# Kernel optimization log

Measured on AMD Instinct MI355X. Metric: run time of the kernel, lower is better.

Reference implementation:

```python
import jax, jax.numpy as jnp
import numpy as np

N = 8192; S = 32; EMB = 256; NH = 8; HD = EMB // NH; NT = 4; K = 2; L = 2; E = 131072
IN_DIMS = [128, 64, 32, 16]; COUNTS = [4096, 2048, 1024, 1024]
BETA = 1.0; TEMPER = 1.0; SLOPE = 0.2; LN_EPS = 1e-5


def setup_inputs() -> dict:
    key = jax.random.key(0)
    ks = iter(jax.random.split(key, 64))
    def nrm(shape, scale=1.0):
        return jax.random.normal(next(ks), shape, jnp.float32) * scale
    inp = {}
    for i, (d, c) in enumerate(zip(IN_DIMS, COUNTS)):
        inp[f"feat{i}"] = nrm((c, d))
        inp[f"Wfc{i}"] = nrm((d, EMB), d ** -0.5)
        inp[f"bfc{i}"] = nrm((EMB,), 0.01)
    inp["type_emb"] = nrm((NT, NT))
    inp["Wgcn"] = nrm((K, EMB, EMB), EMB ** -0.5)
    inp["bgcn"] = nrm((K, EMB), 0.01)
    inp["Wre"] = nrm((K, NT, NT), NT ** -0.5)
    inp["bre"] = nrm((K, NT), 0.01)
    inp["wtre"] = jnp.ones((K, NT), jnp.float32)
    inp["Wl"] = nrm((L, EMB, EMB), EMB ** -0.5)
    inp["Wr"] = nrm((L, EMB, EMB), EMB ** -0.5)
    inp["al"] = nrm((L, HD), HD ** -0.5)
    inp["ar"] = nrm((L, HD), HD ** -0.5)
    inp["Wrs"] = nrm((L, NT, NT * NH), NT ** -0.5)
    inp["Wrt"] = nrm((L, NT, NT * NH), NT ** -0.5)
    inp["Wfin"] = nrm((L, EMB, EMB), EMB ** -0.5)
    inp["ln_g"] = jnp.ones((L, EMB), jnp.float32)
    inp["ln_b"] = jnp.zeros((L, EMB), jnp.float32)
    inp["src"] = jax.random.randint(next(ks), (E,), 0, N)
    inp["dst"] = jax.random.randint(next(ks), (E,), 0, N)
    inp["node_type"] = jnp.concatenate([jnp.full((c,), t, jnp.int32) for t, c in enumerate(COUNTS)])
    inp["seqs"] = jax.random.randint(next(ks), (N, S), 0, N)
    return inp


def _l2n(x):
    return x / jnp.maximum(jnp.linalg.norm(x, axis=1, keepdims=True), 1e-12)


def _ln(x, g, b):
    m = x.mean(-1, keepdims=True)
    v = ((x - m) ** 2).mean(-1, keepdims=True)
    return (x - m) * jax.lax.rsqrt(v + LN_EPS) * g + b


def _agt(h, rh, Wl_, Wr_, al_, ar_, Wrs_, Wrt_, Wfin_, g_, b_):
    B, Sq, _ = h.shape
    fl = (h @ Wl_).reshape(B, Sq, NH, HD).transpose(0, 2, 1, 3)  # [B,NH,S,HD]
    fr = (h @ Wr_).reshape(B, Sq, NH, HD).transpose(0, 2, 1, 3)
    sl = jnp.einsum('bhsd,d->bhs', jax.nn.leaky_relu(fl, SLOPE), al_)
    sr = jnp.einsum('bhsd,d->bhs', jax.nn.leaky_relu(fr, SLOPE), ar_)
    score = sl[:, :, :, None] + sr[:, :, None, :]  # [B,NH,S,S]
    rk = (rh @ Wrs_).reshape(B, Sq, NH, NT).transpose(0, 2, 1, 3)  # [B,NH,S,NT]
    rq = (rh @ Wrt_).reshape(B, Sq, NH, NT).transpose(0, 2, 1, 3)
    score = score + BETA * jnp.einsum('bhir,bhjr->bhij', rk, rq)
    attn = jax.nn.softmax(score / TEMPER, axis=-1)
    ctx = jnp.einsum('bhij,bhjd->bhid', attn, fr)
    h_sa = ctx.transpose(0, 2, 1, 3).reshape(B, Sq, EMB)
    return _ln(h + h_sa @ Wfin_, g_, b_)


def reference(feat0, feat1, feat2, feat3, Wfc0, bfc0, Wfc1, bfc1, Wfc2, bfc2, Wfc3, bfc3,
              type_emb, Wgcn, bgcn, Wre, bre, wtre, Wl, Wr, al, ar, Wrs, Wrt, Wfin, ln_g, ln_b,
              src, dst, node_type, seqs):
    feats = [feat0, feat1, feat2, feat3]
    Wfcs = [Wfc0, Wfc1, Wfc2, Wfc3]
    bfcs = [bfc0, bfc1, bfc2, bfc3]
    gh = jnp.concatenate([f @ W + b for f, W, b in zip(feats, Wfcs, bfcs)], axis=0)  # [N,EMB]
    Nn = gh.shape[0]
    loop = jnp.arange(Nn, dtype=src.dtype)  # self-loops (graph.add_self_loop)
    src_f = jnp.concatenate([src, loop]); dst_f = jnp.concatenate([dst, loop])
    ones = jnp.ones(src_f.shape[0], jnp.float32)
    outdeg = jnp.clip(jax.ops.segment_sum(ones, src_f, num_segments=Nn), 1.0)
    indeg = jnp.clip(jax.ops.segment_sum(ones, dst_f, num_segments=Nn), 1.0)
    n_out = outdeg ** -0.5; n_in = indeg ** -0.5
    ret = [_l2n(gh)]
    R = type_emb[node_type]  # [N,NT]
    for k in range(K):
        # GraphConv, norm='both', relu
        x = (gh * n_out[:, None]) @ Wgcn[k]
        gh = jax.nn.relu(jax.ops.segment_sum(x[src_f], dst_f, num_segments=Nn) * n_in[:, None] + bgcn[k])
        # REConv: left norm, weight, per-node type scale, scatter-sum, right norm, bias, relu
        r = ((R * n_out[:, None]) @ Wre[k]) * wtre[k][node_type][:, None]
        R = jax.nn.relu(jax.ops.segment_sum(r[src_f], dst_f, num_segments=Nn) * n_in[:, None] + bre[k])
    h = gh[seqs]   # [N,S,EMB]
    rh = R[seqs]   # [N,S,NT]
    for l in range(L):
        h = _agt(h, rh, Wl[l], Wr[l], al[l], ar[l], Wrs[l], Wrt[l], Wfin[l], ln_g[l], ln_b[l])
        ret.append(_l2n(h[:, 0, :]))
    return jnp.concatenate(ret, axis=1)  # [N, EMB*(1+L)]
```

## Files before the change

kernel.cpp:

```cpp
#include <hip/hip_runtime.h>
#include <hip/hip_bf16.h>
#include <cstdint>
#include <cstddef>

typedef unsigned short ushortT;
typedef unsigned int uintT;

using bf16x8 = __attribute__((ext_vector_type(8))) short;
using f32x4  = __attribute__((ext_vector_type(4))) float;

static constexpr int NN  = 8192;
static constexpr int EE  = 131072;
static constexpr float SLOPE  = 0.2f;
static constexpr float LN_EPS = 1e-5f;

#define DEVI __device__ __forceinline__

DEVI float red32(float v) {
  #pragma unroll
  for (int m = 16; m >= 1; m >>= 1) v += __shfl_xor(v, m, 64);
  return v;
}
DEVI float red64(float v) {
  #pragma unroll
  for (int m = 32; m >= 1; m >>= 1) v += __shfl_xor(v, m, 64);
  return v;
}
DEVI float max32(float v) {
  #pragma unroll
  for (int m = 16; m >= 1; m >>= 1) v = fmaxf(v, __shfl_xor(v, m, 64));
  return v;
}
DEVI float blo(uintT u) { union { uintT i; float f; } c; c.i = u << 16; return c.f; }
DEVI float bhi(uintT u) { union { uintT i; float f; } c; c.i = u & 0xffff0000u; return c.f; }
DEVI float b2f(ushortT u) { union { uintT i; float f; } c; c.i = ((uintT)u) << 16; return c.f; }
DEVI ushortT f2bu(float f) {
  __hip_bfloat16 h = __float2bfloat16(f);
  return *reinterpret_cast<ushortT*>(&h);
}
DEVI void storeC(float* p, float v) { *p = v; }
DEVI void storeC(ushortT* p, float v) { *p = f2bu(v); }

__global__ __launch_bounds__(256) void fc_kernel(
    const float* __restrict__ f0, const float* __restrict__ f1,
    const float* __restrict__ f2, const float* __restrict__ f3,
    const float* __restrict__ w0, const float* __restrict__ w1,
    const float* __restrict__ w2, const float* __restrict__ w3,
    const float* __restrict__ b0, const float* __restrict__ b1,
    const float* __restrict__ b2, const float* __restrict__ b3,
    float* __restrict__ gh, float* __restrict__ out)
{
  const int nb = blockIdx.x * 32;
  const int t  = threadIdx.x;
  int base, D;
  const float *F, *W, *Bv;
  if (nb < 4096)      { base = 0;    D = 128; F = f0; W = w0; Bv = b0; }
  else if (nb < 6144) { base = 4096; D = 64;  F = f1; W = w1; Bv = b1; }
  else if (nb < 7168) { base = 6144; D = 32;  F = f2; W = w2; Bv = b2; }
  else                { base = 7168; D = 16;  F = f3; W = w3; Bv = b3; }

  __shared__ float Fs[32 * 128];
  __shared__ float red[32][4];
  __shared__ float nrm[32];

  const int total = 32 * D;
  for (int i = t; i < total; i += 256) Fs[i] = F[(size_t)(nb - base) * D + i];
  __syncthreads();

  float acc[32];
  #pragma unroll
  for (int r = 0; r < 32; ++r) acc[r] = Bv[t];
  for (int d = 0; d < D; ++d) {
    float w = W[(size_t)d * 256 + t];
    #pragma unroll
    for (int r = 0; r < 32; ++r) acc[r] = fmaf(Fs[r * D + d], w, acc[r]);
  }

  const int lane = t & 63, wid = t >> 6;
  #pragma unroll
  for (int r = 0; r < 32; ++r) {
    float v = acc[r] * acc[r];
    for (int o = 32; o > 0; o >>= 1) v += __shfl_down(v, o, 64);
    if (lane == 0) red[r][wid] = v;
  }
  __syncthreads();
  if (t < 32) {
    float s = red[t][0] + red[t][1] + red[t][2] + red[t][3];
    nrm[t] = 1.0f / fmaxf(sqrtf(s), 1e-12f);
  }
  __syncthreads();
  #pragma unroll
  for (int r = 0; r < 32; ++r) {
    gh[(size_t)(nb + r) * 256 + t]  = acc[r];
    out[(size_t)(nb + r) * 768 + t] = acc[r] * nrm[r];
  }
}

__global__ __launch_bounds__(256) void zero_counts(int* outc, int* inc) {
  int g = blockIdx.x * 256 + threadIdx.x;
  if (g < NN) outc[g] = 0; else inc[g - NN] = 0;
}
__global__ __launch_bounds__(256) void count_deg(const int* __restrict__ src,
                                                 const int* __restrict__ dst,
                                                 int* outc, int* inc) {
  int g = blockIdx.x * 256 + threadIdx.x;
  atomicAdd(&outc[src[g]], 1);
  atomicAdd(&inc[dst[g]], 1);
}
__global__ __launch_bounds__(256) void norm_kernel(const int* __restrict__ outc,
                                                   const int* __restrict__ inc,
                                                   float* n_out, float* n_in) {
  int g = blockIdx.x * 256 + threadIdx.x;
  n_out[g] = rsqrtf((float)outc[g] + 1.0f);
  n_in[g]  = rsqrtf((float)inc[g] + 1.0f);
}
__global__ __launch_bounds__(1024) void scan_kernel(const int* __restrict__ inc,
                                                    int* __restrict__ offs) {
  __shared__ int sums[1024];
  const int t = threadIdx.x;
  int x[8];
  const int base = t * 8;
  int s = 0;
  #pragma unroll
  for (int i = 0; i < 8; ++i) { int v = inc[base + i] + 1; x[i] = s; s += v; }
  sums[t] = s;
  __syncthreads();
  for (int off = 1; off < 1024; off <<= 1) {
    int a = (t >= off) ? sums[t - off] : 0;
    __syncthreads();
    sums[t] += a;
    __syncthreads();
  }
  const int pre = (t > 0) ? sums[t - 1] : 0;
  #pragma unroll
  for (int i = 0; i < 8; ++i) offs[base + i] = pre + x[i];
  if (t == 1023) offs[NN] = sums[1023];
}
__global__ __launch_bounds__(256) void copy_cur(const int* __restrict__ offs, int* cur) {
  int g = blockIdx.x * 256 + threadIdx.x;
  cur[g] = offs[g];
}
__global__ __launch_bounds__(256) void fill_csr(const int* __restrict__ src,
                                                const int* __restrict__ dst,
                                                int* cur, int* __restrict__ csr) {
  int g = blockIdx.x * 256 + threadIdx.x;
  int s, d;
  if (g < EE) { s = src[g]; d = dst[g]; }
  else        { s = g - EE; d = g - EE; }
  int pos = atomicAdd(&cur[d], 1);
  csr[pos] = s;
}
__global__ __launch_bounds__(256) void init_R(const float* __restrict__ type_emb,
                                              const int* __restrict__ nt,
                                              float* __restrict__ R) {
  int g = blockIdx.x * 256 + threadIdx.x;
  int n = g >> 2, c = g & 3;
  R[g] = type_emb[nt[n] * 4 + c];
}

template<bool ROWSCALE, bool STORE, bool RED, typename CT>
__global__ __launch_bounds__(256) void gemm64_kernel(
    const float* __restrict__ A,
    const float* __restrict__ W,
    const float* __restrict__ rowscale,
    CT* __restrict__ C,
    const float* __restrict__ avec,
    float* __restrict__ SSo)
{
  const int m0 = blockIdx.x * 64;
  const int n0 = blockIdx.y * 64;
  const int t  = threadIdx.x;
  const int tr = t & 15, tc = t >> 4;
  __shared__ alignas(16) float As[32][68];
  __shared__ alignas(16) float Bs[32][68];
  __shared__ float red[64][2];
  float acc[4][4] = {};

  for (int ks = 0; ks < 8; ++ks) {
    const int k0 = ks * 32;
    #pragma unroll
    for (int rep = 0; rep < 8; ++rep) {
      int flat = rep * 256 + t;
      int r = flat >> 5, c = flat & 31;
      As[c][r] = A[(size_t)(m0 + r) * 256 + (k0 + c)];
      int rb = flat >> 6, cb = flat & 63;
      Bs[rb][cb] = W[(size_t)(k0 + rb) * 256 + (n0 + cb)];
    }
    __syncthreads();
    #pragma unroll
    for (int k = 0; k < 32; ++k) {
      const float4 a4 = *reinterpret_cast<const float4*>(&As[k][tr * 4]);
      const float4 b4 = *reinterpret_cast<const float4*>(&Bs[k][tc * 4]);
      const float av[4] = {a4.x, a4.y, a4.z, a4.w};
      const float bv[4] = {b4.x, b4.y, b4.z, b4.w};
      #pragma unroll
      for (int u = 0; u < 4; ++u)
        #pragma unroll
        for (int v = 0; v < 4; ++v)
          acc[u][v] = fmaf(av[u], bv[v], acc[u][v]);
    }
    __syncthreads();
  }

  if constexpr (ROWSCALE) {
    #pragma unroll
    for (int u = 0; u < 4; ++u) {
      float s = rowscale[m0 + tr * 4 + u];
      #pragma unroll
      for (int v = 0; v < 4; ++v) acc[u][v] *= s;
    }
  }
  if constexpr (STORE) {
    #pragma unroll
    for (int u = 0; u < 4; ++u) {
      size_t row = (size_t)(m0 + tr * 4 + u);
      #pragma unroll
      for (int v = 0; v < 4; ++v)
        storeC(&C[row * 256 + (n0 + tc * 4 + v)], acc[u][v]);
    }
  }
  if constexpr (RED) {
    if (t < 128) red[t >> 1][t & 1] = 0.f;
    __syncthreads();
    #pragma unroll
    for (int u = 0; u < 4; ++u) {
      float s = 0.f;
      #pragma unroll
      for (int v = 0; v < 4; ++v) {
        float x = acc[u][v];
        float lr = x > 0.f ? x : SLOPE * x;
        s += lr * avec[(tc * 4 + v) & 31];
      }
      atomicAdd(&red[tr * 4 + u][tc >> 3], s);
    }
    __syncthreads();
    if (t < 128) {
      int r = t >> 1, hh = t & 1;
      SSo[(size_t)(m0 + r) * 8 + blockIdx.y * 2 + hh] = red[r][hh];
    }
  }
}

__global__ __launch_bounds__(256) void mfma_tab_kernel(
    const float* __restrict__ A, const float* __restrict__ W,
    ushortT* __restrict__ C)
{
  const int m0 = blockIdx.x * 64;
  const int n0 = blockIdx.y * 64;
  const int t = threadIdx.x;
  const int w = t >> 6, l = t & 63;
  const int wr = w >> 1, wc = w & 1;
  const int l15 = l & 15, l16 = l >> 4;

  __shared__ alignas(16) ushortT As[64][72];
  __shared__ alignas(16) ushortT Bs[64][72];

  f32x4 acc[2][2];
  #pragma unroll
  for (int mh = 0; mh < 2; ++mh)
    #pragma unroll
    for (int nh = 0; nh < 2; ++nh)
      #pragma unroll
      for (int r = 0; r < 4; ++r) acc[mh][nh][r] = 0.f;

  for (int k0 = 0; k0 < 256; k0 += 64) {
    #pragma unroll
    for (int rep = 0; rep < 16; ++rep) {
      int flat = rep * 256 + t;
      int r = flat >> 6, k = flat & 63;
      As[r][k] = f2bu(A[(size_t)(m0 + r) * 256 + k0 + k]);
    }
    #pragma unroll
    for (int rep = 0; rep < 16; ++rep) {
      int flat = rep * 256 + t;
      int k = flat >> 6, n = flat & 63;
      Bs[n][k] = f2bu(W[(size_t)(k0 + k) * 256 + n0 + n]);
    }
    __syncthreads();
    #pragma unroll
    for (int ks = 0; ks < 2; ++ks) {
      const int kb = ks * 32 + l16 * 8;
      bf16x8 afr[2], bfr[2];
      #pragma unroll
      for (int mh = 0; mh < 2; ++mh)
        afr[mh] = *reinterpret_cast<const bf16x8*>(&As[wr * 32 + mh * 16 + l15][kb]);
      #pragma unroll
      for (int nh = 0; nh < 2; ++nh)
        bfr[nh] = *reinterpret_cast<const bf16x8*>(&Bs[wc * 32 + nh * 16 + l15][kb]);
      #pragma unroll
      for (int mh = 0; mh < 2; ++mh)
        #pragma unroll
        for (int nh = 0; nh < 2; ++nh)
          acc[mh][nh] = __builtin_amdgcn_mfma_f32_16x16x32_bf16(
              afr[mh], bfr[nh], acc[mh][nh], 0, 0, 0);
    }
    __syncthreads();
  }
  #pragma unroll
  for (int mh = 0; mh < 2; ++mh)
    #pragma unroll
    for (int nh = 0; nh < 2; ++nh)
      #pragma unroll
      for (int r = 0; r < 4; ++r) {
        const int row = m0 + wr * 32 + mh * 16 + l16 * 4 + r;
        const int col = n0 + wc * 32 + nh * 16 + l15;
        C[(size_t)row * 256 + col] = f2bu(acc[mh][nh][r]);
      }
}

__global__ __launch_bounds__(256) void agg_kernel(
    const int* __restrict__ offs, const int* __restrict__ csr,
    const float* __restrict__ X, const float* __restrict__ n_in,
    const float* __restrict__ bias, float* __restrict__ ghn)
{
  const int n = blockIdx.x, t = threadIdx.x;
  const int s0 = offs[n], s1 = offs[n + 1];
  float acc = 0.f;
  for (int i = s0; i < s1; ++i) acc += X[(size_t)csr[i] * 256 + t];
  ghn[(size_t)n * 256 + t] = fmaxf(fmaf(acc, n_in[n], bias[t]), 0.f);
}
__global__ __launch_bounds__(256) void re_proj(
    const float* __restrict__ R, const float* __restrict__ n_out,
    const float* __restrict__ Wre, const float* __restrict__ wtre,
    const int* __restrict__ nt, float* __restrict__ rtmp)
{
  int g = blockIdx.x * 256 + threadIdx.x;
  int n = g >> 2, j = g & 3;
  float s = 0.f;
  #pragma unroll
  for (int c = 0; c < 4; ++c) s += R[n * 4 + c] * Wre[c * 4 + j];
  rtmp[g] = s * n_out[n] * wtre[nt[n]];
}
__global__ __launch_bounds__(256) void re_agg(
    const int* __restrict__ offs, const int* __restrict__ csr,
    const float* __restrict__ rtmp, const float* __restrict__ n_in,
    const float* __restrict__ bre, float* __restrict__ Rn)
{
  int g = blockIdx.x * 256 + threadIdx.x;
  int n = g >> 2, j = g & 3;
  float a = 0.f;
  for (int i = offs[n]; i < offs[n + 1]; ++i) a += rtmp[csr[i] * 4 + j];
  Rn[g] = fmaxf(fmaf(a, n_in[n], bre[j]), 0.f);
}
__global__ __launch_bounds__(256) void rkq_kernel(
    const float* __restrict__ R, const float* __restrict__ Wrs,
    const float* __restrict__ Wrt, float* __restrict__ RKQ)
{
  int g = blockIdx.x * 256 + threadIdx.x;
  int n = g >> 7, c = g & 127;
  int which = c >> 5, cc = c & 31;
  const float* Wp = (which == 0) ? Wrs : (which == 1) ? Wrt
                   : (which == 2) ? (Wrs + 128) : (Wrt + 128);
  float s = 0.f;
  #pragma unroll
  for (int r = 0; r < 4; ++r) s += R[n * 4 + r] * Wp[r * 32 + cc];
  RKQ[g] = s;
}

__global__ __launch_bounds__(256) void vec4_kernel(
    const float* __restrict__ ln_g, const float* __restrict__ ln_b,
    const float* __restrict__ Wr2, float* __restrict__ vecs)
{
  const int which = blockIdx.x, t = threadIdx.x;
  const float* s = (which & 1) ? ln_b : ln_g;
  float a = 0.f;
  for (int k = 0; k < 256; ++k) a = fmaf(s[k], Wr2[(size_t)k * 256 + t], a);
  vecs[which * 256 + t] = a;
}
__global__ __launch_bounds__(256) void wg2i_kernel(
    const float* __restrict__ ln_g, const float* __restrict__ Wr2,
    ushortT* __restrict__ Wg2i)
{
  const int gid = blockIdx.x * 256 + threadIdx.x;
  const int ks  = gid >> 10;
  const int cgl = (gid >> 6) & 15;
  const int l   = gid & 63;
  const int col = cgl * 16 + (l & 15);
  const int kb  = ks * 32 + (l >> 4) * 8;
  ushortT v[8];
  #pragma unroll
  for (int e = 0; e < 8; ++e)
    v[e] = f2bu(ln_g[kb + e] * Wr2[(size_t)(kb + e) * 256 + col]);
  *reinterpret_cast<bf16x8*>(&Wg2i[(size_t)gid * 8]) =
      *reinterpret_cast<const bf16x8*>(v);
}
__global__ __launch_bounds__(256) void wl2b_kernel(
    const float* __restrict__ Wl2, ushortT* __restrict__ Wl2b)
{
  int g = blockIdx.x * 256 + threadIdx.x;
  Wl2b[g] = f2bu(Wl2[g]);
}
__global__ __launch_bounds__(256) void ghb_kernel(
    const float* __restrict__ gh, ushortT* __restrict__ ghb)
{
  int g = blockIdx.x * 256 + threadIdx.x;
  ghb[g] = f2bu(gh[g]);
}

__global__ __launch_bounds__(256) void mega7_kernel(
    const int* __restrict__ seqs,
    const ushortT* __restrict__ ghb,
    const ushortT* __restrict__ GW,
    const float* __restrict__ SLg, const float* __restrict__ SRg,
    const float* __restrict__ RKQ,
    const float* __restrict__ vecs,
    const ushortT* __restrict__ Wg2i,
    const ushortT* __restrict__ Wl2b,
    const float* __restrict__ al2, const float* __restrict__ ar2,
    const float* __restrict__ ln_g, const float* __restrict__ ln_b,
    float* __restrict__ h1r0buf, float* __restrict__ ctx2buf,
    float* __restrict__ out)
{
  __shared__ int idx[32];
  __shared__ alignas(16) ushortT bufA[10240];
  __shared__ alignas(16) ushortT bufB[10240];
  __shared__ float SRs[8][32];
  __shared__ float RQs[32][36];
  __shared__ float rk2s[32];
  __shared__ float part[32][4], partq[32][4];
  __shared__ float mu_s[32], rs_s[32];
  __shared__ float SR2s[8][32];
  __shared__ float sl2s[8];
  __shared__ float scp[8][32];
  __shared__ float h1r0s[256];
  __shared__ float wred4[4];
  __shared__ float nrm1s;

  const int b = blockIdx.x, t = threadIdx.x;
  const int h8 = t >> 5, lo = t & 31;
  const int w = t >> 6, l = t & 63;
  const int l15 = l & 15, l16 = l >> 4;

  if (t < 32) idx[t] = seqs[b * 32 + t];
  __syncthreads();

  const float sli = SLg[(size_t)idx[lo] * 8 + h8];
  const float rk0 = RKQ[(size_t)idx[lo] * 128 + h8 * 4 + 0];
  const float rk1 = RKQ[(size_t)idx[lo] * 128 + h8 * 4 + 1];
  const float rk2_ = RKQ[(size_t)idx[lo] * 128 + h8 * 4 + 2];
  const float rk3 = RKQ[(size_t)idx[lo] * 128 + h8 * 4 + 3];

  {
    const uintT* GWu = reinterpret_cast<const uintT*>(GW);
    #pragma unroll
    for (int rep = 0; rep < 16; ++rep) {
      int flat = rep * 256 + t;
      int j = flat >> 7, cp = flat & 127;
      const uintT u = GWu[(size_t)idx[j] * 128 + cp];
      const int rA = 2 * cp;
      const int k = (rA >> 3) & 3;
      const int off = (((j >> 3) ^ k) << 3) + (j & 7);
      bufA[rA * 40 + off]       = (ushortT)(u & 0xffffu);
      bufA[(rA + 1) * 40 + off] = (ushortT)(u >> 16);
    }
  }
  SRs[h8][lo] = SRg[(size_t)idx[lo] * 8 + h8];
  #pragma unroll
  for (int rep = 0; rep < 4; ++rep) {
    int flat = rep * 256 + t, s3 = flat >> 5, c3 = flat & 31;
    RQs[s3][c3] = RKQ[(size_t)idx[s3] * 128 + 32 + c3];
  }
  if (t < 32) rk2s[t] = RKQ[(size_t)idx[0] * 128 + 64 + t];
  __syncthreads();

  {
    float p1[32];
    float m = -1e30f;
    #pragma unroll
    for (int j = 0; j < 32; ++j) {
      float sc = sli + SRs[h8][j]
               + rk0 * RQs[j][h8 * 4 + 0] + rk1 * RQs[j][h8 * 4 + 1]
               + rk2_ * RQs[j][h8 * 4 + 2] + rk3 * RQs[j][h8 * 4 + 3];
      p1[j] = sc; m = fmaxf(m, sc);
    }
    float sum = 0.f;
    #pragma unroll
    for (int j = 0; j < 32; ++j) { p1[j] = __expf(p1[j] - m); sum += p1[j]; }
    const float inv = 1.f / sum;
    const int row = t;
    const int k = (row >> 3) & 3;
    uintT* pw = reinterpret_cast<uintT*>(bufB) + row * 20;
    #pragma unroll
    for (int o = 0; o < 4; ++o) {
      uint4 v;
      v.x = (uintT)f2bu(p1[8 * o + 0] * inv) | ((uintT)f2bu(p1[8 * o + 1] * inv) << 16);
      v.y = (uintT)f2bu(p1[8 * o + 2] * inv) | ((uintT)f2bu(p1[8 * o + 3] * inv) << 16);
      v.z = (uintT)f2bu(p1[8 * o + 4] * inv) | ((uintT)f2bu(p1[8 * o + 5] * inv) << 16);
      v.w = (uintT)f2bu(p1[8 * o + 6] * inv) | ((uintT)f2bu(p1[8 * o + 7] * inv) << 16);
      *reinterpret_cast<uint4*>(pw + ((o ^ k) << 2)) = v;
    }
  }
  __syncthreads();

  int irow[2][4];
  #pragma unroll
  for (int mh = 0; mh < 2; ++mh)
    #pragma unroll
    for (int r = 0; r < 4; ++r)
      irow[mh][r] = idx[mh * 16 + l16 * 4 + r];

  bf16x8 af[2][2];
  #pragma unroll
  for (int hh = 0; hh < 2; ++hh) {
    const int h = 2 * w + hh;
    #pragma unroll
    for (int mh = 0; mh < 2; ++mh) {
      const int row = h * 32 + mh * 16 + l15;
      const int k = (row >> 3) & 3;
      af[hh][mh] = *reinterpret_cast<const bf16x8*>(&bufB[row * 40 + ((l16 ^ k) << 3)]);
    }
  }

  f32x4 acc[2][2][2];
  #pragma unroll
  for (int hh = 0; hh < 2; ++hh) {
    const int h = 2 * w + hh;
    bf16x8 bf[2];
    #pragma unroll
    for (int nh = 0; nh < 2; ++nh) {
      const int row = h * 32 + nh * 16 + l15;
      const int k = (row >> 3) & 3;
      bf[nh] = *reinterpret_cast<const bf16x8*>(&bufA[row * 40 + ((l16 ^ k) << 3)]);
    }
    #pragma unroll
    for (int mh = 0; mh < 2; ++mh)
      #pragma unroll
      for (int nh = 0; nh < 2; ++nh) {
        f32x4 z = {0.f, 0.f, 0.f, 0.f};
        acc[hh][mh][nh] = __builtin_amdgcn_mfma_f32_16x16x32_bf16(af[hh][mh], bf[nh], z, 0, 0, 0);
      }
  }
  {
    float sum_[2][4], sq_[2][4];
    #pragma unroll
    for (int mh = 0; mh < 2; ++mh)
      #pragma unroll
      for (int r = 0; r < 4; ++r) { sum_[mh][r] = 0.f; sq_[mh][r] = 0.f; }
    #pragma unroll
    for (int hh = 0; hh < 2; ++hh)
      #pragma unroll
      for (int mh = 0; mh < 2; ++mh)
        #pragma unroll
        for (int nh = 0; nh < 2; ++nh) {
          const int col = (2 * w + hh) * 32 + nh * 16 + l15;
          #pragma unroll
          for (int r = 0; r < 4; ++r) {
            float v = acc[hh][mh][nh][r] + b2f(ghb[(size_t)irow[mh][r] * 256 + col]);
            acc[hh][mh][nh][r] = v;
            sum_[mh][r] += v;
            sq_[mh][r] = fmaf(v, v, sq_[mh][r]);
          }
        }
    #pragma unroll
    for (int mh = 0; mh < 2; ++mh)
      #pragma unroll
      for (int r = 0; r < 4; ++r) {
        float s = sum_[mh][r], q = sq_[mh][r];
        #pragma unroll
        for (int m = 8; m >= 1; m >>= 1) {
          s += __shfl_xor(s, m, 64);
          q += __shfl_xor(q, m, 64);
        }
        if (l15 == 0) {
          part[mh * 16 + l16 * 4 + r][w]  = s;
          partq[mh * 16 + l16 * 4 + r][w] = q;
        }
      }
    if (l16 == 0) {
      #pragma unroll
      for (int hh = 0; hh < 2; ++hh)
        #pragma unroll
        for (int nh = 0; nh < 2; ++nh)
          h1r0s[(2 * w + hh) * 32 + nh * 16 + l15] = acc[hh][0][nh][0];
    }
  }
  __syncthreads();

  if (t < 32) {
    float sm = part[t][0] + part[t][1] + part[t][2] + part[t][3];
    float sq = partq[t][0] + partq[t][1] + partq[t][2] + partq[t][3];
    const float m = sm * (1.f / 256.f);
    const float v = fmaxf(sq * (1.f / 256.f) - m * m, 0.f);
    mu_s[t] = m;
    rs_s[t] = rsqrtf(v + LN_EPS);
  }
  __syncthreads();

  #pragma unroll
  for (int hh = 0; hh < 2; ++hh)
    #pragma unroll
    for (int mh = 0; mh < 2; ++mh)
      #pragma unroll
      for (int nh = 0; nh < 2; ++nh) {
        const int col = (2 * w + hh) * 32 + nh * 16 + l15;
        #pragma unroll
        for (int r = 0; r < 4; ++r) {
          const int row = mh * 16 + l16 * 4 + r;
          bufB[row * 264 + col] = f2bu(acc[hh][mh][nh][r]);
        }
      }
  #pragma unroll
  for (int rep = 0; rep < 4; ++rep) {
    int flat = rep * 256 + t, s3 = flat >> 5, c3 = flat & 31;
    RQs[s3][c3] = RKQ[(size_t)idx[s3] * 128 + 96 + c3];
  }
  {
    const float mu0 = mu_s[0], rs0 = rs_s[0];
    float hv = fmaf((h1r0s[t] - mu0) * rs0, ln_g[t], ln_b[t]);
    h1r0buf[(size_t)b * 256 + t] = hv;
    float sq = red64(hv * hv);
    h1r0s[t] = hv;
    if ((t & 63) == 0) wred4[t >> 6] = sq;
  }
  __syncthreads();

  if (t == 0) nrm1s = 1.f / fmaxf(sqrtf(wred4[0] + wred4[1] + wred4[2] + wred4[3]), 1e-12f);

  {
    f32x4 acc2[2][4];
    #pragma unroll
    for (int mh = 0; mh < 2; ++mh)
      #pragma unroll
      for (int cg = 0; cg < 4; ++cg)
        #pragma unroll
        for (int r = 0; r < 4; ++r) acc2[mh][cg][r] = 0.f;
    #pragma unroll
    for (int ks = 0; ks < 8; ++ks) {
      const int ko = ks * 32 + l16 * 8;
      bf16x8 a2[2];
      #pragma unroll
      for (int mh = 0; mh < 2; ++mh)
        a2[mh] = *reinterpret_cast<const bf16x8*>(&bufB[(mh * 16 + l15) * 264 + ko]);
      #pragma unroll
      for (int cg = 0; cg < 4; ++cg) {
        const bf16x8 b2 = *reinterpret_cast<const bf16x8*>(
            &Wg2i[((size_t)(ks * 16 + (w * 4 + cg)) * 64 + l) * 8]);
        #pragma unroll
        for (int mh = 0; mh < 2; ++mh)
          acc2[mh][cg] = __builtin_amdgcn_mfma_f32_16x16x32_bf16(a2[mh], b2, acc2[mh][cg], 0, 0, 0);
      }
    }
    float rsv[2][4], rmv[2][4];
    #pragma unroll
    for (int mh = 0; mh < 2; ++mh)
      #pragma unroll
      for (int r = 0; r < 4; ++r) {
        const int row = mh * 16 + l16 * 4 + r;
        rsv[mh][r] = rs_s[row];
        rmv[mh][r] = rsv[mh][r] * mu_s[row];
      }
    float sacc[2][2][4];
    #pragma unroll
    for (int hh = 0; hh < 2; ++hh)
      #pragma unroll
      for (int mh = 0; mh < 2; ++mh)
        #pragma unroll
        for (int r = 0; r < 4; ++r) sacc[hh][mh][r] = 0.f;
    float ar2v[2] = { ar2[l15], ar2[16 + l15] };
    #pragma unroll
    for (int cg = 0; cg < 4; ++cg) {
      const int col = w * 64 + cg * 16 + l15;
      const float v1c = vecs[col], v2c = vecs[256 + col];
      const int hh = cg >> 1;
      #pragma unroll
      for (int mh = 0; mh < 2; ++mh)
        #pragma unroll
        for (int r = 0; r < 4; ++r) {
          const int row = mh * 16 + l16 * 4 + r;
          float fa = fmaf(rsv[mh][r], acc2[mh][cg][r], fmaf(-rmv[mh][r], v1c, v2c));
          bufA[row * 268 + col] = f2bu(fa);
          float lr = fa > 0.f ? fa : SLOPE * fa;
          sacc[hh][mh][r] = fmaf(lr, ar2v[cg & 1], sacc[hh][mh][r]);
        }
    }
    #pragma unroll
    for (int hh = 0; hh < 2; ++hh)
      #pragma unroll
      for (int mh = 0; mh < 2; ++mh)
        #pragma unroll
        for (int r = 0; r < 4; ++r) {
          float s = sacc[hh][mh][r];
          #pragma unroll
          for (int m = 8; m >= 1; m >>= 1) s += __shfl_xor(s, m, 64);
          if (l15 == 0) SR2s[2 * w + hh][mh * 16 + l16 * 4 + r] = s;
        }
  }
  {
    float fl = 0.f;
    #pragma unroll 8
    for (int k = 0; k < 256; ++k)
      fl = fmaf(h1r0s[k], b2f(Wl2b[(size_t)k * 256 + t]), fl);
    float lr = (fl > 0.f ? fl : SLOPE * fl) * al2[lo];
    lr = red32(lr);
    if (lo == 0) sl2s[h8] = lr;
  }
  __syncthreads();

  {
    float s2 = sl2s[h8] + SR2s[h8][lo]
             + rk2s[h8 * 4 + 0] * RQs[lo][h8 * 4 + 0]
             + rk2s[h8 * 4 + 1] * RQs[lo][h8 * 4 + 1]
             + rk2s[h8 * 4 + 2] * RQs[lo][h8 * 4 + 2]
             + rk2s[h8 * 4 + 3] * RQs[lo][h8 * 4 + 3];
    const float m2 = max32(s2);
    const float e = __expf(s2 - m2);
    const float su = red32(e);
    scp[h8][lo] = e / su;
  }
  __syncthreads();

  {
    float a = 0.f;
    #pragma unroll
    for (int j = 0; j < 32; ++j) a = fmaf(scp[h8][j], b2f(bufA[j * 268 + t]), a);
    ctx2buf[(size_t)b * 256 + t] = a;
  }
  out[(size_t)b * 768 + 256 + t] = h1r0s[t] * nrm1s;
}

__global__ __launch_bounds__(256) void final_ln_kernel(
    const float* __restrict__ A,
    const float* __restrict__ W,
    const float* __restrict__ res,
    const float* __restrict__ lng, const float* __restrict__ lnb,
    float* __restrict__ out)
{
  const int m0 = blockIdx.x * 64;
  const int t  = threadIdx.x;
  const int tr = t & 15, tc = t >> 4;
  __shared__ alignas(16) float As[32][68];
  __shared__ alignas(16) float Bs[32][264];
  __shared__ float red[64][16];
  __shared__ float stat[64];
  float acc[4][16] = {};

  for (int ks = 0; ks < 8; ++ks) {
    const int k0 = ks * 32;
    #pragma unroll
    for (int rep = 0; rep < 8; ++rep) {
      int flat = rep * 256 + t;
      int r = flat >> 5, c = flat & 31;
      As[c][r] = A[(size_t)(m0 + r) * 256 + (k0 + c)];
    }
    #pragma unroll
    for (int rep = 0; rep < 32; ++rep) {
      int flat = rep * 256 + t;
      int rb = flat >> 8, cb = flat & 255;
      Bs[rb][cb] = W[(size_t)(k0 + rb) * 256 + cb];
    }
    __syncthreads();
    #pragma unroll
    for (int k = 0; k < 32; ++k) {
      const float4 a4 = *reinterpret_cast<const float4*>(&As[k][tr * 4]);
      const float av[4] = {a4.x, a4.y, a4.z, a4.w};
      #pragma unroll
      for (int q = 0; q < 4; ++q) {
        const float4 b4 = *reinterpret_cast<const float4*>(&Bs[k][tc * 16 + q * 4]);
        const float bv[4] = {b4.x, b4.y, b4.z, b4.w};
        #pragma unroll
        for (int u = 0; u < 4; ++u)
          #pragma unroll
          for (int v = 0; v < 4; ++v)
            acc[u][q * 4 + v] = fmaf(av[u], bv[v], acc[u][q * 4 + v]);
      }
    }
    __syncthreads();
  }

  int rows[4];
  #pragma unroll
  for (int u = 0; u < 4; ++u) rows[u] = m0 + tr * 4 + u;

  #pragma unroll
  for (int u = 0; u < 4; ++u) {
    const float* rp = &res[(size_t)rows[u] * 256 + tc * 16];
    #pragma unroll
    for (int v = 0; v < 16; ++v) acc[u][v] += rp[v];
  }
  #pragma unroll
  for (int u = 0; u < 4; ++u) {
    float s = 0.f;
    #pragma unroll
    for (int v = 0; v < 16; ++v) s += acc[u][v];
    red[tr * 4 + u][tc] = s;
  }
  __syncthreads();
  if (t < 64) {
    float s = 0.f;
    #pragma unroll
    for (int g = 0; g < 16; ++g) s += red[t][g];
    stat[t] = s * (1.0f / 256.0f);
  }
  __syncthreads();
  float mu[4];
  #pragma unroll
  for (int u = 0; u < 4; ++u) mu[u] = stat[tr * 4 + u];
  #pragma unroll
  for (int u = 0; u < 4; ++u) {
    float s = 0.f;
    #pragma unroll
    for (int v = 0; v < 16; ++v) { float d = acc[u][v] - mu[u]; s += d * d; }
    red[tr * 4 + u][tc] = s;
  }
  __syncthreads();
  if (t < 64) {
    float s = 0.f;
    #pragma unroll
    for (int g = 0; g < 16; ++g) s += red[t][g];
    stat[t] = rsqrtf(s * (1.0f / 256.0f) + LN_EPS);
  }
  __syncthreads();
  float rst[4];
  #pragma unroll
  for (int u = 0; u < 4; ++u) rst[u] = stat[tr * 4 + u];
  #pragma unroll
  for (int u = 0; u < 4; ++u) {
    float s = 0.f;
    #pragma unroll
    for (int v = 0; v < 16; ++v) {
      int col = tc * 16 + v;
      float yv = fmaf((acc[u][v] - mu[u]) * rst[u], lng[col], lnb[col]);
      acc[u][v] = yv;
      s += yv * yv;
    }
    red[tr * 4 + u][tc] = s;
  }
  __syncthreads();
  if (t < 64) {
    float s = 0.f;
    #pragma unroll
    for (int g = 0; g < 16; ++g) s += red[t][g];
    stat[t] = 1.0f / fmaxf(sqrtf(s), 1e-12f);
  }
  __syncthreads();
  #pragma unroll
  for (int u = 0; u < 4; ++u) {
    float rn = stat[tr * 4 + u];
    #pragma unroll
    for (int v = 0; v < 16; ++v)
      out[(size_t)rows[u] * 768 + 512 + tc * 16 + v] = acc[u][v] * rn;
  }
}

extern "C" void kernel_launch(void* const* d_in, const int* in_sizes, int n_in,
                              void* d_out, int out_size, void* d_ws, size_t ws_size,
                              hipStream_t stream)
{
  (void)in_sizes; (void)n_in; (void)out_size; (void)ws_size;

  const float* feat[4]; const float* wfc[4]; const float* bfc[4];
  for (int i = 0; i < 4; ++i) {
    feat[i] = (const float*)d_in[i * 3 + 0];
    wfc[i]  = (const float*)d_in[i * 3 + 1];
    bfc[i]  = (const float*)d_in[i * 3 + 2];
  }
  const float* type_emb = (const float*)d_in[12];
  const float* Wgcn = (const float*)d_in[13];
  const float* bgcn = (const float*)d_in[14];
  const float* Wre  = (const float*)d_in[15];
  const float* bre  = (const float*)d_in[16];
  const float* wtre = (const float*)d_in[17];
  const float* Wl   = (const float*)d_in[18];
  const float* Wr   = (const float*)d_in[19];
  const float* al   = (const float*)d_in[20];
  const float* ar   = (const float*)d_in[21];
  const float* Wrs  = (const float*)d_in[22];
  const float* Wrt  = (const float*)d_in[23];
  const float* Wfin = (const float*)d_in[24];
  const float* ln_g = (const float*)d_in[25];
  const float* ln_b = (const float*)d_in[26];
  const int* src       = (const int*)d_in[27];
  const int* dst       = (const int*)d_in[28];
  const int* node_type = (const int*)d_in[29];
  const int* seqs      = (const int*)d_in[30];
  float* out = (float*)d_out;

  char* p = (char*)d_ws;
  auto take = [&](size_t n) { char* q = p; p += (n + 255) & ~(size_t)255; return q; };
  float* gh    = (float*)take((size_t)NN * 256 * 4);
  float* Xbuf  = (float*)take((size_t)NN * 256 * 4);
  float* GR1   = (float*)take((size_t)NN * 256 * 4);
  float* RKQ   = (float*)take((size_t)NN * 128 * 4);
  float* SLg   = (float*)take((size_t)NN * 8 * 4);
  float* SRg   = (float*)take((size_t)NN * 8 * 4);
  float* n_out = (float*)take((size_t)NN * 4);
  float* n_in_ = (float*)take((size_t)NN * 4);
  int*   outc  = (int*)take((size_t)NN * 4);
  int*   inc   = (int*)take((size_t)NN * 4);
  int*   offs  = (int*)take((size_t)(NN + 1) * 4);
  int*   cur   = (int*)take((size_t)NN * 4);
  int*   csr   = (int*)take((size_t)(EE + NN) * 4);
  float* R     = (float*)take((size_t)NN * 4 * 4);
  float* rtmp  = (float*)take((size_t)NN * 4 * 4);
  ushortT* GW   = (ushortT*)take((size_t)NN * 256 * 2);
  ushortT* ghb  = (ushortT*)take((size_t)NN * 256 * 2);
  ushortT* Wg2i = (ushortT*)take((size_t)131072 * 2);
  ushortT* Wl2b = (ushortT*)take((size_t)65536 * 2);
  float* vecs  = (float*)take((size_t)2 * 256 * 4);
  float* ctx2buf = Xbuf;
  float* h1r0buf = GR1;

  const float* Wr2 = Wr + 65536;
  const float* Wl2 = Wl + 65536;

  fc_kernel<<<256, 256, 0, stream>>>(feat[0], feat[1], feat[2], feat[3],
                                     wfc[0], wfc[1], wfc[2], wfc[3],
                                     bfc[0], bfc[1], bfc[2], bfc[3], gh, out);
  zero_counts<<<64, 256, 0, stream>>>(outc, inc);
  count_deg<<<512, 256, 0, stream>>>(src, dst, outc, inc);
  norm_kernel<<<32, 256, 0, stream>>>(outc, inc, n_out, n_in_);
  scan_kernel<<<1, 1024, 0, stream>>>(inc, offs);
  copy_cur<<<32, 256, 0, stream>>>(offs, cur);
  fill_csr<<<544, 256, 0, stream>>>(src, dst, cur, csr);
  init_R<<<128, 256, 0, stream>>>(type_emb, node_type, R);

  vec4_kernel<<<2, 256, 0, stream>>>(ln_g, ln_b, Wr2, vecs);
  wg2i_kernel<<<64, 256, 0, stream>>>(ln_g, Wr2, Wg2i);
  wl2b_kernel<<<256, 256, 0, stream>>>(Wl2, Wl2b);

  for (int k = 0; k < 2; ++k) {
    gemm64_kernel<true, true, false, float>
        <<<dim3(128, 4), 256, 0, stream>>>(gh, Wgcn + (size_t)k * 65536,
                                           n_out, Xbuf, nullptr, nullptr);
    agg_kernel<<<NN, 256, 0, stream>>>(offs, csr, Xbuf, n_in_, bgcn + k * 256, gh);
    re_proj<<<128, 256, 0, stream>>>(R, n_out, Wre + k * 16, wtre + k * 4, node_type, rtmp);
    re_agg<<<128, 256, 0, stream>>>(offs, csr, rtmp, n_in_, bre + k * 4, R);
  }

  rkq_kernel<<<4096, 256, 0, stream>>>(R, Wrs, Wrt, RKQ);
  gemm64_kernel<false, false, true, float>
      <<<dim3(128, 4), 256, 0, stream>>>(gh, Wl, nullptr, (float*)nullptr, al, SLg);
  gemm64_kernel<false, true, true, float>
      <<<dim3(128, 4), 256, 0, stream>>>(gh, Wr, nullptr, GR1, ar, SRg);
  mfma_tab_kernel<<<dim3(128, 4), 256, 0, stream>>>(GR1, Wfin, GW);
  ghb_kernel<<<NN, 256, 0, stream>>>(gh, ghb);

  mega7_kernel<<<NN, 256, 0, stream>>>(seqs, ghb, GW, SLg, SRg, RKQ, vecs,
                                       Wg2i, Wl2b,
                                       al + 32, ar + 32, ln_g, ln_b,
                                       h1r0buf, ctx2buf, out);

  final_ln_kernel<<<128, 256, 0, stream>>>(ctx2buf, Wfin + 65536, h1r0buf,
                                           ln_g + 256, ln_b + 256, out);
}
```

Baseline: 573.3 us.

## Replace fp32 SIMT GEMMs with shared bf16 MFMA GEMM and split final LayerNorm

The scalar fp32 64x64 GEMM kernel is replaced by one templated bf16 MFMA GEMM. Its template options cover row scaling, storing and the leaky-relu attention-score reduction, and it now serves the GCN projections, the Wl/Wr projections and the Wfin table. The fused fp32 final GEMM+LayerNorm+L2-norm kernel becomes an MFMA GEMM writing to a scratch buffer, followed by a per-row LN/L2 kernel. The aim is to use matrix cores instead of FMA loops, at the cost of bf16 rounding of inputs in more GEMMs and one extra intermediate round trip to memory. Variance is now computed as E[x^2]-mu^2.

```diff
diff --git a/kernel.cpp b/kernel.cpp
--- a/kernel.cpp
+++ b/kernel.cpp
@@ -159,91 +159,11 @@
 }
 
 template<bool ROWSCALE, bool STORE, bool RED, typename CT>
-__global__ __launch_bounds__(256) void gemm64_kernel(
-    const float* __restrict__ A,
-    const float* __restrict__ W,
+__global__ __launch_bounds__(256) void mfma_gemm_kernel(
+    const float* __restrict__ A, const float* __restrict__ W,
     const float* __restrict__ rowscale,
-    CT* __restrict__ C,
-    const float* __restrict__ avec,
+    CT* __restrict__ C, const float* __restrict__ avec,
     float* __restrict__ SSo)
-{
-  const int m0 = blockIdx.x * 64;
-  const int n0 = blockIdx.y * 64;
-  const int t  = threadIdx.x;
-  const int tr = t & 15, tc = t >> 4;
-  __shared__ alignas(16) float As[32][68];
-  __shared__ alignas(16) float Bs[32][68];
-  __shared__ float red[64][2];
-  float acc[4][4] = {};
-
-  for (int ks = 0; ks < 8; ++ks) {
-    const int k0 = ks * 32;
-    #pragma unroll
-    for (int rep = 0; rep < 8; ++rep) {
-      int flat = rep * 256 + t;
-      int r = flat >> 5, c = flat & 31;
-      As[c][r] = A[(size_t)(m0 + r) * 256 + (k0 + c)];
-      int rb = flat >> 6, cb = flat & 63;
-      Bs[rb][cb] = W[(size_t)(k0 + rb) * 256 + (n0 + cb)];
-    }
-    __syncthreads();
-    #pragma unroll
-    for (int k = 0; k < 32; ++k) {
-      const float4 a4 = *reinterpret_cast<const float4*>(&As[k][tr * 4]);
-      const float4 b4 = *reinterpret_cast<const float4*>(&Bs[k][tc * 4]);
-      const float av[4] = {a4.x, a4.y, a4.z, a4.w};
-      const float bv[4] = {b4.x, b4.y, b4.z, b4.w};
-      #pragma unroll
-      for (int u = 0; u < 4; ++u)
-        #pragma unroll
-        for (int v = 0; v < 4; ++v)
-          acc[u][v] = fmaf(av[u], bv[v], acc[u][v]);
-    }
-    __syncthreads();
-  }
-
-  if constexpr (ROWSCALE) {
-    #pragma unroll
-    for (int u = 0; u < 4; ++u) {
-      float s = rowscale[m0 + tr * 4 + u];
-      #pragma unroll
-      for (int v = 0; v < 4; ++v) acc[u][v] *= s;
-    }
-  }
-  if constexpr (STORE) {
-    #pragma unroll
-    for (int u = 0; u < 4; ++u) {
-      size_t row = (size_t)(m0 + tr * 4 + u);
-      #pragma unroll
-      for (int v = 0; v < 4; ++v)
-        storeC(&C[row * 256 + (n0 + tc * 4 + v)], acc[u][v]);
-    }
-  }
-  if constexpr (RED) {
-    if (t < 128) red[t >> 1][t & 1] = 0.f;
-    __syncthreads();
-    #pragma unroll
-    for (int u = 0; u < 4; ++u) {
-      float s = 0.f;
-      #pragma unroll
-      for (int v = 0; v < 4; ++v) {
-        float x = acc[u][v];
-        float lr = x > 0.f ? x : SLOPE * x;
-        s += lr * avec[(tc * 4 + v) & 31];
-      }
-      atomicAdd(&red[tr * 4 + u][tc >> 3], s);
-    }
-    __syncthreads();
-    if (t < 128) {
-      int r = t >> 1, hh = t & 1;
-      SSo[(size_t)(m0 + r) * 8 + blockIdx.y * 2 + hh] = red[r][hh];
-    }
-  }
-}
-
-__global__ __launch_bounds__(256) void mfma_tab_kernel(
-    const float* __restrict__ A, const float* __restrict__ W,
-    ushortT* __restrict__ C)
 {
   const int m0 = blockIdx.x * 64;
   const int n0 = blockIdx.y * 64;
@@ -268,7 +188,9 @@
     for (int rep = 0; rep < 16; ++rep) {
       int flat = rep * 256 + t;
       int r = flat >> 6, k = flat & 63;
-      As[r][k] = f2bu(A[(size_t)(m0 + r) * 256 + k0 + k]);
+      float v = A[(size_t)(m0 + r) * 256 + k0 + k];
+      if constexpr (ROWSCALE) v *= rowscale[m0 + r];
+      As[r][k] = f2bu(v);
     }
     #pragma unroll
     for (int rep = 0; rep < 16; ++rep) {
@@ -296,16 +218,39 @@
     }
     __syncthreads();
   }
-  #pragma unroll
-  for (int mh = 0; mh < 2; ++mh)
-    #pragma unroll
-    for (int nh = 0; nh < 2; ++nh)
+  if constexpr (STORE) {
+    #pragma unroll
+    for (int mh = 0; mh < 2; ++mh)
+      #pragma unroll
+      for (int nh = 0; nh < 2; ++nh)
+        #pragma unroll
+        for (int r = 0; r < 4; ++r) {
+          const int row = m0 + wr * 32 + mh * 16 + l16 * 4 + r;
+          const int col = n0 + wc * 32 + nh * 16 + l15;
+          storeC(&C[(size_t)row * 256 + col], acc[mh][nh][r]);
+        }
+  }
+  if constexpr (RED) {
+    const float av0 = avec[l15], av1 = avec[16 + l15];
+    #pragma unroll
+    for (int mh = 0; mh < 2; ++mh)
       #pragma unroll
       for (int r = 0; r < 4; ++r) {
-        const int row = m0 + wr * 32 + mh * 16 + l16 * 4 + r;
-        const int col = n0 + wc * 32 + nh * 16 + l15;
-        C[(size_t)row * 256 + col] = f2bu(acc[mh][nh][r]);
+        float s = 0.f;
+        {
+          float x = acc[mh][0][r];
+          s = fmaf(x > 0.f ? x : SLOPE * x, av0, s);
+          x = acc[mh][1][r];
+          s = fmaf(x > 0.f ? x : SLOPE * x, av1, s);
+        }
+        #pragma unroll
+        for (int m = 8; m >= 1; m >>= 1) s += __shfl_xor(s, m, 64);
+        if (l15 == 0) {
+          const int row = m0 + wr * 32 + mh * 16 + l16 * 4 + r;
+          SSo[(size_t)row * 8 + blockIdx.y * 2 + wc] = s;
+        }
       }
+  }
 }
 
 __global__ __launch_bounds__(256) void agg_kernel(
@@ -718,128 +663,28 @@
   out[(size_t)b * 768 + 256 + t] = h1r0s[t] * nrm1s;
 }
 
-__global__ __launch_bounds__(256) void final_ln_kernel(
-    const float* __restrict__ A,
-    const float* __restrict__ W,
-    const float* __restrict__ res,
+__global__ __launch_bounds__(256) void ln_l2n_kernel(
+    const float* __restrict__ Y, const float* __restrict__ res,
     const float* __restrict__ lng, const float* __restrict__ lnb,
     float* __restrict__ out)
 {
-  const int m0 = blockIdx.x * 64;
-  const int t  = threadIdx.x;
-  const int tr = t & 15, tc = t >> 4;
-  __shared__ alignas(16) float As[32][68];
-  __shared__ alignas(16) float Bs[32][264];
-  __shared__ float red[64][16];
-  __shared__ float stat[64];
-  float acc[4][16] = {};
-
-  for (int ks = 0; ks < 8; ++ks) {
-    const int k0 = ks * 32;
-    #pragma unroll
-    for (int rep = 0; rep < 8; ++rep) {
-      int flat = rep * 256 + t;
-      int r = flat >> 5, c = flat & 31;
-      As[c][r] = A[(size_t)(m0 + r) * 256 + (k0 + c)];
-    }
-    #pragma unroll
-    for (int rep = 0; rep < 32; ++rep) {
-      int flat = rep * 256 + t;
-      int rb = flat >> 8, cb = flat & 255;
-      Bs[rb][cb] = W[(size_t)(k0 + rb) * 256 + cb];
-    }
-    __syncthreads();
-    #pragma unroll
-    for (int k = 0; k < 32; ++k) {
-      const float4 a4 = *reinterpret_cast<const float4*>(&As[k][tr * 4]);
-      const float av[4] = {a4.x, a4.y, a4.z, a4.w};
-      #pragma unroll
-      for (int q = 0; q < 4; ++q) {
-        const float4 b4 = *reinterpret_cast<const float4*>(&Bs[k][tc * 16 + q * 4]);
-        const float bv[4] = {b4.x, b4.y, b4.z, b4.w};
-        #pragma unroll
-        for (int u = 0; u < 4; ++u)
-          #pragma unroll
-          for (int v = 0; v < 4; ++v)
-            acc[u][q * 4 + v] = fmaf(av[u], bv[v], acc[u][q * 4 + v]);
-      }
-    }
-    __syncthreads();
-  }
-
-  int rows[4];
-  #pragma unroll
-  for (int u = 0; u < 4; ++u) rows[u] = m0 + tr * 4 + u;
-
-  #pragma unroll
-  for (int u = 0; u < 4; ++u) {
-    const float* rp = &res[(size_t)rows[u] * 256 + tc * 16];
-    #pragma unroll
-    for (int v = 0; v < 16; ++v) acc[u][v] += rp[v];
-  }
-  #pragma unroll
-  for (int u = 0; u < 4; ++u) {
-    float s = 0.f;
-    #pragma unroll
-    for (int v = 0; v < 16; ++v) s += acc[u][v];
-    red[tr * 4 + u][tc] = s;
-  }
-  __syncthreads();
-  if (t < 64) {
-    float s = 0.f;
-    #pragma unroll
-    for (int g = 0; g < 16; ++g) s += red[t][g];
-    stat[t] = s * (1.0f / 256.0f);
-  }
-  __syncthreads();
-  float mu[4];
-  #pragma unroll
-  for (int u = 0; u < 4; ++u) mu[u] = stat[tr * 4 + u];
-  #pragma unroll
-  for (int u = 0; u < 4; ++u) {
-    float s = 0.f;
-    #pragma unroll
-    for (int v = 0; v < 16; ++v) { float d = acc[u][v] - mu[u]; s += d * d; }
-    red[tr * 4 + u][tc] = s;
-  }
-  __syncthreads();
-  if (t < 64) {
-    float s = 0.f;
-    #pragma unroll
-    for (int g = 0; g < 16; ++g) s += red[t][g];
-    stat[t] = rsqrtf(s * (1.0f / 256.0f) + LN_EPS);
-  }
-  __syncthreads();
-  float rst[4];
-  #pragma unroll
-  for (int u = 0; u < 4; ++u) rst[u] = stat[tr * 4 + u];
-  #pragma unroll
-  for (int u = 0; u < 4; ++u) {
-    float s = 0.f;
-    #pragma unroll
-    for (int v = 0; v < 16; ++v) {
-      int col = tc * 16 + v;
-      float yv = fmaf((acc[u][v] - mu[u]) * rst[u], lng[col], lnb[col]);
-      acc[u][v] = yv;
-      s += yv * yv;
-    }
-    red[tr * 4 + u][tc] = s;
-  }
-  __syncthreads();
-  if (t < 64) {
-    float s = 0.f;
-    #pragma unroll
-    for (int g = 0; g < 16; ++g) s += red[t][g];
-    stat[t] = 1.0f / fmaxf(sqrtf(s), 1e-12f);
-  }
-  __syncthreads();
-  #pragma unroll
-  for (int u = 0; u < 4; ++u) {
-    float rn = stat[tr * 4 + u];
-    #pragma unroll
-    for (int v = 0; v < 16; ++v)
-      out[(size_t)rows[u] * 768 + 512 + tc * 16 + v] = acc[u][v] * rn;
-  }
+  const int row = blockIdx.x, t = threadIdx.x;
+  __shared__ float s4[4], q4[4];
+  const float y = Y[(size_t)row * 256 + t] + res[(size_t)row * 256 + t];
+  float s = red64(y);
+  float q = red64(y * y);
+  if ((t & 63) == 0) { s4[t >> 6] = s; q4[t >> 6] = q; }
+  __syncthreads();
+  const float mu = (s4[0] + s4[1] + s4[2] + s4[3]) * (1.f / 256.f);
+  const float var = fmaxf((q4[0] + q4[1] + q4[2] + q4[3]) * (1.f / 256.f) - mu * mu, 0.f);
+  const float rstd = rsqrtf(var + LN_EPS);
+  const float yn = fmaf((y - mu) * rstd, lng[t], lnb[t]);
+  float nq = red64(yn * yn);
+  __syncthreads();
+  if ((t & 63) == 0) s4[t >> 6] = nq;
+  __syncthreads();
+  const float nrm = 1.f / fmaxf(sqrtf(s4[0] + s4[1] + s4[2] + s4[3]), 1e-12f);
+  out[(size_t)row * 768 + 512 + t] = yn * nrm;
 }
 
 extern "C" void kernel_launch(void* const* d_in, const int* in_sizes, int n_in,
@@ -899,6 +744,7 @@
   float* vecs  = (float*)take((size_t)2 * 256 * 4);
   float* ctx2buf = Xbuf;
   float* h1r0buf = GR1;
+  float* Yb      = gh;
 
   const float* Wr2 = Wr + 65536;
   const float* Wl2 = Wl + 65536;
@@ -919,7 +765,7 @@
   wl2b_kernel<<<256, 256, 0, stream>>>(Wl2, Wl2b);
 
   for (int k = 0; k < 2; ++k) {
-    gemm64_kernel<true, true, false, float>
+    mfma_gemm_kernel<true, true, false, float>
         <<<dim3(128, 4), 256, 0, stream>>>(gh, Wgcn + (size_t)k * 65536,
                                            n_out, Xbuf, nullptr, nullptr);
     agg_kernel<<<NN, 256, 0, stream>>>(offs, csr, Xbuf, n_in_, bgcn + k * 256, gh);
@@ -928,11 +774,12 @@
   }
 
   rkq_kernel<<<4096, 256, 0, stream>>>(R, Wrs, Wrt, RKQ);
-  gemm64_kernel<false, false, true, float>
+  mfma_gemm_kernel<false, false, true, float>
       <<<dim3(128, 4), 256, 0, stream>>>(gh, Wl, nullptr, (float*)nullptr, al, SLg);
-  gemm64_kernel<false, true, true, float>
+  mfma_gemm_kernel<false, true, true, float>
       <<<dim3(128, 4), 256, 0, stream>>>(gh, Wr, nullptr, GR1, ar, SRg);
-  mfma_tab_kernel<<<dim3(128, 4), 256, 0, stream>>>(GR1, Wfin, GW);
+  mfma_gemm_kernel<false, true, false, ushortT>
+      <<<dim3(128, 4), 256, 0, stream>>>(GR1, Wfin, nullptr, GW, nullptr, nullptr);
   ghb_kernel<<<NN, 256, 0, stream>>>(gh, ghb);
 
   mega7_kernel<<<NN, 256, 0, stream>>>(seqs, ghb, GW, SLg, SRg, RKQ, vecs,
@@ -940,6 +787,8 @@
                                        al + 32, ar + 32, ln_g, ln_b,
                                        h1r0buf, ctx2buf, out);
 
-  final_ln_kernel<<<128, 256, 0, stream>>>(ctx2buf, Wfin + 65536, h1r0buf,
-                                           ln_g + 256, ln_b + 256, out);
-}
+  mfma_gemm_kernel<false, true, false, float>
+      <<<dim3(128, 4), 256, 0, stream>>>(ctx2buf, Wfin + 65536, nullptr,
+                                         Yb, nullptr, nullptr);
+  ln_l2n_kernel<<<NN, 256, 0, stream>>>(Yb, h1r0buf, ln_g + 256, ln_b + 256, out);
+}
```

After: 584.2 us. Within noise of the previous version (+1.9%).
